# Kernel tuning notes

Hardware: AMD Instinct MI355X
Metric: run time of the kernel (lower is better)

The kernel has to match this reference:

```python
import jax, jax.numpy as jnp
import numpy as np

N_NODES = 100000
N_EDGES = 1600000
NFEAT = 512
HIDDEN = 128
NCLASS = 40


def setup_inputs() -> dict:
    key = jax.random.key(0)
    ks = jax.random.split(key, 8)
    x = jax.random.normal(ks[0], (N_NODES, NFEAT), dtype=jnp.float32)
    edge_src = jax.random.randint(ks[1], (N_EDGES,), 0, N_NODES, dtype=jnp.int32)
    edge_dst = jax.random.randint(ks[2], (N_EDGES,), 0, N_NODES, dtype=jnp.int32)
    # normalized adjacency values (D^-1/2 A D^-1/2 style), all positive
    edge_val = jax.random.uniform(ks[3], (N_EDGES,), dtype=jnp.float32)
    # glorot-ish init like pygcn's reset_parameters
    W1 = jax.random.normal(ks[4], (NFEAT, HIDDEN), dtype=jnp.float32) / np.sqrt(NFEAT)
    b1 = jnp.zeros((HIDDEN,), dtype=jnp.float32)
    W2 = jax.random.normal(ks[5], (HIDDEN, NCLASS), dtype=jnp.float32) / np.sqrt(HIDDEN)
    b2 = jnp.zeros((NCLASS,), dtype=jnp.float32)
    return {"x": x, "edge_src": edge_src, "edge_dst": edge_dst, "edge_val": edge_val,
            "W1": W1, "b1": b1, "W2": W2, "b2": b2}


def _gcn_layer(h, edge_src, edge_dst, edge_val, W, b):
    # support = h @ W ; out = spmm(adj, support) + b
    support = h @ W                                  # [N, d_out]
    msg = support[edge_src] * edge_val[:, None]      # [E, d_out] gather
    agg = jax.ops.segment_sum(msg, edge_dst, num_segments=N_NODES)  # scatter-add
    return agg + b


def reference(x, edge_src, edge_dst, edge_val, W1, b1, W2, b2):
    h = _gcn_layer(x, edge_src, edge_dst, edge_val, W1, b1)
    h = jax.nn.relu(h)
    # dropout=0.0 -> branch skipped (faithful to `if self.dropout:` with falsy value)
    h = _gcn_layer(h, edge_src, edge_dst, edge_val, W2, b2)
    return jax.nn.log_softmax(h, axis=1)
```

## Files before the change

kernel.cpp:

```cpp
#include <hip/hip_runtime.h>
#include <stdint.h>

#define NN 100000
#define NE 1600000
#define NF 512
#define NH 128
#define NC 40
#define BKT 64
#define DEGS 16
#define NGB 782

typedef float f32x4 __attribute__((ext_vector_type(4)));
typedef short bf16x8 __attribute__((ext_vector_type(8)));

__device__ __forceinline__ unsigned short f2bf(float f){
    unsigned u = __float_as_uint(f);
    u = u + 0x7FFFu + ((u >> 16) & 1u);
    return (unsigned short)(u >> 16);
}
__device__ __forceinline__ unsigned pk2(float a, float b){
    return (unsigned)f2bf(a) | ((unsigned)f2bf(b) << 16);
}
__device__ __forceinline__ float blo(unsigned u){ return __uint_as_float(u << 16); }
__device__ __forceinline__ float bhi(unsigned u){ return __uint_as_float(u & 0xffff0000u); }

__global__ __launch_bounds__(256) void wprep(const float* __restrict__ W1, const float* __restrict__ W2,
                                             unsigned short* __restrict__ W1t, unsigned short* __restrict__ W2t){
    int tid = blockIdx.x * 256 + threadIdx.x;
    if (tid < NF * NH){
        int c = tid >> 9;
        int k = tid & 511;
        W1t[c * NF + k] = f2bf(W1[k * NH + c]);
    }
    int t2 = tid - NF * NH;
    if (t2 >= 0 && t2 < 48 * NH){
        int c = t2 >> 7;
        int k = t2 & 127;
        W2t[c * NH + k] = (c < NC) ? f2bf(W2[k * NC + c]) : (unsigned short)0;
    }
}

__global__ __launch_bounds__(256, 3) void gemm1_edge(const float* __restrict__ x,
                                                     const unsigned short* __restrict__ W1t,
                                                     unsigned short* __restrict__ s1,
                                                     const int* __restrict__ esrc,
                                                     const int* __restrict__ edst,
                                                     const float* __restrict__ eval,
                                                     int* __restrict__ deg, int2* __restrict__ pk){
    __shared__ unsigned short Al[2][128 * 40];
    __shared__ unsigned short Bl[2][128 * 40];
    if (blockIdx.x >= NGB){
        int tid = (blockIdx.x - NGB) * 256 + threadIdx.x;
        if (tid < NE){
            int d = edst[tid];
            int pos = atomicAdd(&deg[d * DEGS], 1);
            if (pos < BKT)
                pk[(size_t)d * BKT + pos] = make_int2(esrc[tid], __float_as_int(eval[tid]));
        }
        return;
    }
    const int tid  = threadIdx.x;
    const int wid  = tid >> 6;
    const int lane = tid & 63;
    const int quad = lane >> 4;
    const int l15  = lane & 15;
    const int br   = blockIdx.x * 128;

    const int r    = tid >> 1;
    const int half = tid & 1;

    int arow = br + r; if (arow >= NN) arow = NN - 1;
    const float* aptr = x + (size_t)arow * NF + half * 16;
    const unsigned short* bptr = W1t + (size_t)r * NF + half * 16;

    float4 pa0, pa1, pa2, pa3;
    uint4  pb0, pb1;
    {
        const float4* ap = (const float4*)aptr;
        pa0 = ap[0]; pa1 = ap[1]; pa2 = ap[2]; pa3 = ap[3];
        const uint4* bp = (const uint4*)bptr;
        pb0 = bp[0]; pb1 = bp[1];
        unsigned* Ad = (unsigned*)&Al[0][r * 40 + half * 16];
        Ad[0] = pk2(pa0.x, pa0.y); Ad[1] = pk2(pa0.z, pa0.w);
        Ad[2] = pk2(pa1.x, pa1.y); Ad[3] = pk2(pa1.z, pa1.w);
        Ad[4] = pk2(pa2.x, pa2.y); Ad[5] = pk2(pa2.z, pa2.w);
        Ad[6] = pk2(pa3.x, pa3.y); Ad[7] = pk2(pa3.z, pa3.w);
        uint4* Bd = (uint4*)&Bl[0][r * 40 + half * 16];
        Bd[0] = pb0; Bd[1] = pb1;
    }
    __syncthreads();

    f32x4 acc[2][8];
#pragma unroll
    for (int i = 0; i < 2; i++)
#pragma unroll
        for (int j = 0; j < 8; j++) acc[i][j] = (f32x4){0.f, 0.f, 0.f, 0.f};

    int cur = 0;
    for (int ks = 0; ks < NF; ks += 32){
        const bool more = (ks + 32 < NF);
        if (more){
            const float4* ap = (const float4*)(aptr + ks + 32);
            pa0 = ap[0]; pa1 = ap[1]; pa2 = ap[2]; pa3 = ap[3];
            const uint4* bp = (const uint4*)(bptr + ks + 32);
            pb0 = bp[0]; pb1 = bp[1];
        }

        bf16x8 a0 = *(const bf16x8*)&Al[cur][(wid * 32 +      l15) * 40 + quad * 8];
        bf16x8 a1 = *(const bf16x8*)&Al[cur][(wid * 32 + 16 + l15) * 40 + quad * 8];
        bf16x8 bb[8];
#pragma unroll
        for (int ct = 0; ct < 8; ct++)
            bb[ct] = *(const bf16x8*)&Bl[cur][(ct * 16 + l15) * 40 + quad * 8];
#pragma unroll
        for (int ct = 0; ct < 8; ct++){
            acc[0][ct] = __builtin_amdgcn_mfma_f32_16x16x32_bf16(a0, bb[ct], acc[0][ct], 0, 0, 0);
            acc[1][ct] = __builtin_amdgcn_mfma_f32_16x16x32_bf16(a1, bb[ct], acc[1][ct], 0, 0, 0);
        }

        if (more){
            int nxt = cur ^ 1;
            unsigned* Ad = (unsigned*)&Al[nxt][r * 40 + half * 16];
            Ad[0] = pk2(pa0.x, pa0.y); Ad[1] = pk2(pa0.z, pa0.w);
            Ad[2] = pk2(pa1.x, pa1.y); Ad[3] = pk2(pa1.z, pa1.w);
            Ad[4] = pk2(pa2.x, pa2.y); Ad[5] = pk2(pa2.z, pa2.w);
            Ad[6] = pk2(pa3.x, pa3.y); Ad[7] = pk2(pa3.z, pa3.w);
            uint4* Bd = (uint4*)&Bl[nxt][r * 40 + half * 16];
            Bd[0] = pb0; Bd[1] = pb1;
        }
        __syncthreads();
        cur ^= 1;
    }

#pragma unroll
    for (int rt = 0; rt < 2; rt++)
#pragma unroll
        for (int ct = 0; ct < 8; ct++)
#pragma unroll
            for (int i = 0; i < 4; i++){
                int row = br + wid * 32 + rt * 16 + quad * 4 + i;
                if (row < NN) s1[(size_t)row * NH + ct * 16 + l15] = f2bf(acc[rt][ct][i]);
            }
}

__global__ __launch_bounds__(256) void agg1(const uint4* __restrict__ s1v,
                                            const int* __restrict__ deg,
                                            const int2* __restrict__ pk,
                                            const float* __restrict__ b1, uint4* __restrict__ h){
    const int lane  = threadIdx.x & 63;
    const int quad  = lane >> 4;
    const int hl    = lane & 15;
    const int lbase = quad * 16;
    const int node  = blockIdx.x * 16 + (threadIdx.x >> 6) * 4 + quad;

    const int s = node * BKT;
    int dg = deg[node * DEGS]; if (dg > BKT) dg = BKT;
    const int e = s + dg;
    float a[8];
#pragma unroll
    for (int t = 0; t < 8; t++) a[t] = 0.f;

    int2 rec = make_int2(0, 0);
    {
        int c0 = e - s; if (c0 > 16) c0 = 16;
        if (hl < c0) rec = pk[s + hl];
    }
    for (int base = s; base < e; base += 16){
        int cnt = e - base; if (cnt > 16) cnt = 16;
        int2 cur = rec;
        int nb = base + 16;
        if (nb < e){
            int cn = e - nb; if (cn > 16) cn = 16;
            rec = make_int2(0, 0);
            if (hl < cn) rec = pk[nb + hl];
        }
        int j = 0;
        for (; j + 8 <= cnt; j += 8){
            int is[8];
#pragma unroll
            for (int q = 0; q < 8; q++) is[q] = __shfl(cur.x, lbase + j + q, 64);
            uint4 us[8];
#pragma unroll
            for (int q = 0; q < 8; q++) us[q] = s1v[(size_t)is[q] * 16 + hl];
            float vs[8];
#pragma unroll
            for (int q = 0; q < 8; q++) vs[q] = __int_as_float(__shfl(cur.y, lbase + j + q, 64));
#pragma unroll
            for (int q = 0; q < 8; q++){
                float v = vs[q];
                a[0] += v * blo(us[q].x); a[1] += v * bhi(us[q].x);
                a[2] += v * blo(us[q].y); a[3] += v * bhi(us[q].y);
                a[4] += v * blo(us[q].z); a[5] += v * bhi(us[q].z);
                a[6] += v * blo(us[q].w); a[7] += v * bhi(us[q].w);
            }
        }
        for (; j < cnt; j++){
            int   i0 = __shfl(cur.x, lbase + j, 64);
            float v0 = __int_as_float(__shfl(cur.y, lbase + j, 64));
            uint4 u  = s1v[(size_t)i0 * 16 + hl];
            a[0] += v0 * blo(u.x); a[1] += v0 * bhi(u.x);
            a[2] += v0 * blo(u.y); a[3] += v0 * bhi(u.y);
            a[4] += v0 * blo(u.z); a[5] += v0 * bhi(u.z);
            a[6] += v0 * blo(u.w); a[7] += v0 * bhi(u.w);
        }
    }
    const float4* b1v = (const float4*)b1;
    float4 bA = b1v[2 * hl], bB = b1v[2 * hl + 1];
    a[0] += bA.x; a[1] += bA.y; a[2] += bA.z; a[3] += bA.w;
    a[4] += bB.x; a[5] += bB.y; a[6] += bB.z; a[7] += bB.w;
#pragma unroll
    for (int t = 0; t < 8; t++) a[t] = fmaxf(a[t], 0.f);
    h[(size_t)node * 16 + hl] = make_uint4(pk2(a[0], a[1]), pk2(a[2], a[3]),
                                           pk2(a[4], a[5]), pk2(a[6], a[7]));
}

__global__ __launch_bounds__(256) void gemm2(const unsigned short* __restrict__ h,
                                             const unsigned short* __restrict__ W2t,
                                             unsigned short* __restrict__ s2p){
    const int tid  = threadIdx.x;
    const int wid  = tid >> 6;
    const int lane = tid & 63;
    const int quad = lane >> 4;
    const int l15  = lane & 15;
    const int row0 = blockIdx.x * 64 + wid * 16;

    bf16x8 bf[3][4];
#pragma unroll
    for (int ct = 0; ct < 3; ct++)
#pragma unroll
        for (int ks = 0; ks < 4; ks++)
            bf[ct][ks] = *(const bf16x8*)&W2t[(ct * 16 + l15) * NH + ks * 32 + quad * 8];

    int arow = row0 + l15; if (arow >= NN) arow = NN - 1;
    const unsigned short* ap = h + (size_t)arow * NH;

    bf16x8 a[4];
#pragma unroll
    for (int ks = 0; ks < 4; ks++) a[ks] = *(const bf16x8*)&ap[ks * 32 + quad * 8];

    f32x4 acc[3];
#pragma unroll
    for (int ct = 0; ct < 3; ct++) acc[ct] = (f32x4){0.f, 0.f, 0.f, 0.f};
#pragma unroll
    for (int ks = 0; ks < 4; ks++)
#pragma unroll
        for (int ct = 0; ct < 3; ct++)
            acc[ct] = __builtin_amdgcn_mfma_f32_16x16x32_bf16(a[ks], bf[ct][ks], acc[ct], 0, 0, 0);

#pragma unroll
    for (int ct = 0; ct < 3; ct++)
#pragma unroll
        for (int i = 0; i < 4; i++){
            int row = row0 + quad * 4 + i;
            if (row < NN) s2p[(size_t)row * 64 + ct * 16 + l15] = f2bf(acc[ct][i]);
        }
}

__global__ __launch_bounds__(256) void agg2(const uint4* __restrict__ s2v,
                                            const int* __restrict__ deg,
                                            const int2* __restrict__ pk,
                                            const float* __restrict__ b2, float* __restrict__ out){
    const int lane  = threadIdx.x & 63;
    const int oct   = lane >> 3;
    const int hl    = lane & 7;
    const int lbase = oct * 8;
    const int node  = blockIdx.x * 32 + (threadIdx.x >> 6) * 8 + oct;

    const int s = node * BKT;
    int dg = deg[node * DEGS]; if (dg > BKT) dg = BKT;
    const int e = s + dg;
    float a[8];
#pragma unroll
    for (int t = 0; t < 8; t++) a[t] = 0.f;

    int2 rec = make_int2(0, 0);
    {
        int c0 = e - s; if (c0 > 8) c0 = 8;
        if (hl < c0) rec = pk[s + hl];
    }
    for (int base = s; base < e; base += 8){
        int cnt = e - base; if (cnt > 8) cnt = 8;
        int2 cur = rec;
        int nb = base + 8;
        if (nb < e){
            int cn = e - nb; if (cn > 8) cn = 8;
            rec = make_int2(0, 0);
            if (hl < cn) rec = pk[nb + hl];
        }
        if (cnt == 8){
            int is[8];
#pragma unroll
            for (int q = 0; q < 8; q++) is[q] = __shfl(cur.x, lbase + q, 64);
            uint4 us[8];
#pragma unroll
            for (int q = 0; q < 8; q++) us[q] = s2v[(size_t)is[q] * 8 + hl];
            float vs[8];
#pragma unroll
            for (int q = 0; q < 8; q++) vs[q] = __int_as_float(__shfl(cur.y, lbase + q, 64));
#pragma unroll
            for (int q = 0; q < 8; q++){
                float v = vs[q];
                a[0] += v * blo(us[q].x); a[1] += v * bhi(us[q].x);
                a[2] += v * blo(us[q].y); a[3] += v * bhi(us[q].y);
                a[4] += v * blo(us[q].z); a[5] += v * bhi(us[q].z);
                a[6] += v * blo(us[q].w); a[7] += v * bhi(us[q].w);
            }
        } else {
            for (int j = 0; j < cnt; j++){
                int   i0 = __shfl(cur.x, lbase + j, 64);
                float v0 = __int_as_float(__shfl(cur.y, lbase + j, 64));
                uint4 u  = s2v[(size_t)i0 * 8 + hl];
                a[0] += v0 * blo(u.x); a[1] += v0 * bhi(u.x);
                a[2] += v0 * blo(u.y); a[3] += v0 * bhi(u.y);
                a[4] += v0 * blo(u.z); a[5] += v0 * bhi(u.z);
                a[6] += v0 * blo(u.w); a[7] += v0 * bhi(u.w);
            }
        }
    }
    const bool act = hl < 5;
    float z[8];
    if (act){
        const float4* b2v = (const float4*)b2;
        float4 cA = b2v[2 * hl], cB = b2v[2 * hl + 1];
        z[0] = a[0] + cA.x; z[1] = a[1] + cA.y; z[2] = a[2] + cA.z; z[3] = a[3] + cA.w;
        z[4] = a[4] + cB.x; z[5] = a[5] + cB.y; z[6] = a[6] + cB.z; z[7] = a[7] + cB.w;
    } else {
#pragma unroll
        for (int t = 0; t < 8; t++) z[t] = -INFINITY;
    }
    float m = z[0];
#pragma unroll
    for (int t = 1; t < 8; t++) m = fmaxf(m, z[t]);
#pragma unroll
    for (int o = 4; o; o >>= 1) m = fmaxf(m, __shfl_xor(m, o, 8));
    float pe = 0.f;
    if (act){
#pragma unroll
        for (int t = 0; t < 8; t++) pe += __expf(z[t] - m);
    }
#pragma unroll
    for (int o = 4; o; o >>= 1) pe += __shfl_xor(pe, o, 8);
    if (act){
        float l = __logf(pe) + m;
        float* op = out + (size_t)node * NC + 8 * hl;
        *(float4*)op       = make_float4(z[0] - l, z[1] - l, z[2] - l, z[3] - l);
        *(float4*)(op + 4) = make_float4(z[4] - l, z[5] - l, z[6] - l, z[7] - l);
    }
}

extern "C" void kernel_launch(void* const* d_in, const int* in_sizes, int n_in,
                              void* d_out, int out_size, void* d_ws, size_t ws_size,
                              hipStream_t stream) {
    const float* x    = (const float*)d_in[0];
    const int*   esrc = (const int*)  d_in[1];
    const int*   edst = (const int*)  d_in[2];
    const float* eval = (const float*)d_in[3];
    const float* W1   = (const float*)d_in[4];
    const float* b1   = (const float*)d_in[5];
    const float* W2   = (const float*)d_in[6];
    const float* b2   = (const float*)d_in[7];
    float* out = (float*)d_out;

    char* ws = (char*)d_ws;
    size_t off = 0;
    auto alloc = [&](size_t bytes) -> void* {
        void* p = ws + off;
        off += (bytes + 255) & ~(size_t)255;
        return p;
    };
    unsigned short* W1t  = (unsigned short*)alloc((size_t)NF * NH * 2);
    unsigned short* W2t  = (unsigned short*)alloc((size_t)48 * NH * 2);
    unsigned short* s1   = (unsigned short*)alloc((size_t)NN * NH * 2);
    unsigned short* h    = (unsigned short*)alloc((size_t)NN * NH * 2);
    unsigned short* s2p  = (unsigned short*)alloc((size_t)NN * 64 * 2);
    int*   deg   = (int*)  alloc((size_t)NN * DEGS * 4);
    int2*  pk    = (int2*) alloc((size_t)NN * BKT * 8);

    hipMemsetAsync(deg, 0, (size_t)NN * DEGS * 4, stream);

    wprep     <<<280, 256, 0, stream>>>(W1, W2, W1t, W2t);
    gemm1_edge<<<NGB + (NE + 255) / 256, 256, 0, stream>>>(x, W1t, s1, esrc, edst, eval, deg, pk);
    agg1      <<<NN / 16, 256, 0, stream>>>((const uint4*)s1, deg, pk, b1, (uint4*)h);
    gemm2     <<<(NN + 63) / 64, 256, 0, stream>>>(h, W2t, s2p);
    agg2      <<<NN / 32, 256, 0, stream>>>((const uint4*)s2p, deg, pk, b2, out);
}
```

Measured before the change: 501.6 us.

## Fuse layer-1 aggregation with layer-2 GEMM through shared memory

Merges the agg1 and gemm2 kernels. Each block now aggregates 64 nodes in four passes, keeps the ReLU'd bf16 hidden rows in an LDS tile, and then runs the MFMA projection against W2 directly from that tile. This drops the global write and re-read of the 100000x128 hidden matrix and one kernel launch. In exchange, blocks cover 4x more nodes, so there are fewer blocks and less parallelism for the latency-bound gather, plus a block barrier before the GEMM.

```diff
diff --git a/kernel.cpp b/kernel.cpp
--- a/kernel.cpp
+++ b/kernel.cpp
@@ -143,100 +143,102 @@
             }
 }
 
-__global__ __launch_bounds__(256) void agg1(const uint4* __restrict__ s1v,
-                                            const int* __restrict__ deg,
-                                            const int2* __restrict__ pk,
-                                            const float* __restrict__ b1, uint4* __restrict__ h){
-    const int lane  = threadIdx.x & 63;
+__global__ __launch_bounds__(256) void agg1g2(const uint4* __restrict__ s1v,
+                                              const int* __restrict__ deg,
+                                              const int2* __restrict__ pk,
+                                              const float* __restrict__ b1,
+                                              const unsigned short* __restrict__ W2t,
+                                              unsigned short* __restrict__ s2p){
+    __shared__ unsigned short Hl[64][136];
+    const int tid   = threadIdx.x;
+    const int wid   = tid >> 6;
+    const int lane  = tid & 63;
     const int quad  = lane >> 4;
     const int hl    = lane & 15;
     const int lbase = quad * 16;
-    const int node  = blockIdx.x * 16 + (threadIdx.x >> 6) * 4 + quad;
-
-    const int s = node * BKT;
-    int dg = deg[node * DEGS]; if (dg > BKT) dg = BKT;
-    const int e = s + dg;
-    float a[8];
-#pragma unroll
-    for (int t = 0; t < 8; t++) a[t] = 0.f;
-
-    int2 rec = make_int2(0, 0);
-    {
-        int c0 = e - s; if (c0 > 16) c0 = 16;
-        if (hl < c0) rec = pk[s + hl];
-    }
-    for (int base = s; base < e; base += 16){
-        int cnt = e - base; if (cnt > 16) cnt = 16;
-        int2 cur = rec;
-        int nb = base + 16;
-        if (nb < e){
-            int cn = e - nb; if (cn > 16) cn = 16;
-            rec = make_int2(0, 0);
-            if (hl < cn) rec = pk[nb + hl];
-        }
-        int j = 0;
-        for (; j + 8 <= cnt; j += 8){
-            int is[8];
-#pragma unroll
-            for (int q = 0; q < 8; q++) is[q] = __shfl(cur.x, lbase + j + q, 64);
-            uint4 us[8];
-#pragma unroll
-            for (int q = 0; q < 8; q++) us[q] = s1v[(size_t)is[q] * 16 + hl];
-            float vs[8];
-#pragma unroll
-            for (int q = 0; q < 8; q++) vs[q] = __int_as_float(__shfl(cur.y, lbase + j + q, 64));
-#pragma unroll
-            for (int q = 0; q < 8; q++){
-                float v = vs[q];
-                a[0] += v * blo(us[q].x); a[1] += v * bhi(us[q].x);
-                a[2] += v * blo(us[q].y); a[3] += v * bhi(us[q].y);
-                a[4] += v * blo(us[q].z); a[5] += v * bhi(us[q].z);
-                a[6] += v * blo(us[q].w); a[7] += v * bhi(us[q].w);
-            }
-        }
-        for (; j < cnt; j++){
-            int   i0 = __shfl(cur.x, lbase + j, 64);
-            float v0 = __int_as_float(__shfl(cur.y, lbase + j, 64));
-            uint4 u  = s1v[(size_t)i0 * 16 + hl];
-            a[0] += v0 * blo(u.x); a[1] += v0 * bhi(u.x);
-            a[2] += v0 * blo(u.y); a[3] += v0 * bhi(u.y);
-            a[4] += v0 * blo(u.z); a[5] += v0 * bhi(u.z);
-            a[6] += v0 * blo(u.w); a[7] += v0 * bhi(u.w);
-        }
-    }
+    const int nb    = blockIdx.x * 64;
+
     const float4* b1v = (const float4*)b1;
-    float4 bA = b1v[2 * hl], bB = b1v[2 * hl + 1];
-    a[0] += bA.x; a[1] += bA.y; a[2] += bA.z; a[3] += bA.w;
-    a[4] += bB.x; a[5] += bB.y; a[6] += bB.z; a[7] += bB.w;
-#pragma unroll
-    for (int t = 0; t < 8; t++) a[t] = fmaxf(a[t], 0.f);
-    h[(size_t)node * 16 + hl] = make_uint4(pk2(a[0], a[1]), pk2(a[2], a[3]),
-                                           pk2(a[4], a[5]), pk2(a[6], a[7]));
-}
-
-__global__ __launch_bounds__(256) void gemm2(const unsigned short* __restrict__ h,
-                                             const unsigned short* __restrict__ W2t,
-                                             unsigned short* __restrict__ s2p){
-    const int tid  = threadIdx.x;
-    const int wid  = tid >> 6;
-    const int lane = tid & 63;
-    const int quad = lane >> 4;
-    const int l15  = lane & 15;
-    const int row0 = blockIdx.x * 64 + wid * 16;
+    const float4 bA = b1v[2 * hl], bB = b1v[2 * hl + 1];
+
+#pragma unroll
+    for (int pass = 0; pass < 4; pass++){
+        const int nloc = pass * 16 + wid * 4 + quad;
+        const int node = nb + nloc;
+        float a[8];
+#pragma unroll
+        for (int t = 0; t < 8; t++) a[t] = 0.f;
+
+        if (node < NN){
+            const int s = node * BKT;
+            int dg = deg[node * DEGS]; if (dg > BKT) dg = BKT;
+            const int e = s + dg;
+
+            int2 rec = make_int2(0, 0);
+            {
+                int c0 = e - s; if (c0 > 16) c0 = 16;
+                if (hl < c0) rec = pk[s + hl];
+            }
+            for (int base = s; base < e; base += 16){
+                int cnt = e - base; if (cnt > 16) cnt = 16;
+                int2 cur = rec;
+                int nxb = base + 16;
+                if (nxb < e){
+                    int cn = e - nxb; if (cn > 16) cn = 16;
+                    rec = make_int2(0, 0);
+                    if (hl < cn) rec = pk[nxb + hl];
+                }
+                int j = 0;
+                for (; j + 8 <= cnt; j += 8){
+                    int is[8];
+#pragma unroll
+                    for (int q = 0; q < 8; q++) is[q] = __shfl(cur.x, lbase + j + q, 64);
+                    uint4 us[8];
+#pragma unroll
+                    for (int q = 0; q < 8; q++) us[q] = s1v[(size_t)is[q] * 16 + hl];
+                    float vs[8];
+#pragma unroll
+                    for (int q = 0; q < 8; q++) vs[q] = __int_as_float(__shfl(cur.y, lbase + j + q, 64));
+#pragma unroll
+                    for (int q = 0; q < 8; q++){
+                        float v = vs[q];
+                        a[0] += v * blo(us[q].x); a[1] += v * bhi(us[q].x);
+                        a[2] += v * blo(us[q].y); a[3] += v * bhi(us[q].y);
+                        a[4] += v * blo(us[q].z); a[5] += v * bhi(us[q].z);
+                        a[6] += v * blo(us[q].w); a[7] += v * bhi(us[q].w);
+                    }
+                }
+                for (; j < cnt; j++){
+                    int   i0 = __shfl(cur.x, lbase + j, 64);
+                    float v0 = __int_as_float(__shfl(cur.y, lbase + j, 64));
+                    uint4 u  = s1v[(size_t)i0 * 16 + hl];
+                    a[0] += v0 * blo(u.x); a[1] += v0 * bhi(u.x);
+                    a[2] += v0 * blo(u.y); a[3] += v0 * bhi(u.y);
+                    a[4] += v0 * blo(u.z); a[5] += v0 * bhi(u.z);
+                    a[6] += v0 * blo(u.w); a[7] += v0 * bhi(u.w);
+                }
+            }
+            a[0] += bA.x; a[1] += bA.y; a[2] += bA.z; a[3] += bA.w;
+            a[4] += bB.x; a[5] += bB.y; a[6] += bB.z; a[7] += bB.w;
+#pragma unroll
+            for (int t = 0; t < 8; t++) a[t] = fmaxf(a[t], 0.f);
+        }
+        *(uint4*)&Hl[nloc][hl * 8] = make_uint4(pk2(a[0], a[1]), pk2(a[2], a[3]),
+                                                pk2(a[4], a[5]), pk2(a[6], a[7]));
+    }
+    __syncthreads();
 
     bf16x8 bf[3][4];
 #pragma unroll
     for (int ct = 0; ct < 3; ct++)
 #pragma unroll
         for (int ks = 0; ks < 4; ks++)
-            bf[ct][ks] = *(const bf16x8*)&W2t[(ct * 16 + l15) * NH + ks * 32 + quad * 8];
-
-    int arow = row0 + l15; if (arow >= NN) arow = NN - 1;
-    const unsigned short* ap = h + (size_t)arow * NH;
-
-    bf16x8 a[4];
-#pragma unroll
-    for (int ks = 0; ks < 4; ks++) a[ks] = *(const bf16x8*)&ap[ks * 32 + quad * 8];
+            bf[ct][ks] = *(const bf16x8*)&W2t[(ct * 16 + hl) * NH + ks * 32 + quad * 8];
+
+    bf16x8 af[4];
+#pragma unroll
+    for (int ks = 0; ks < 4; ks++)
+        af[ks] = *(const bf16x8*)&Hl[wid * 16 + hl][ks * 32 + quad * 8];
 
     f32x4 acc[3];
 #pragma unroll
@@ -245,14 +247,14 @@
     for (int ks = 0; ks < 4; ks++)
 #pragma unroll
         for (int ct = 0; ct < 3; ct++)
-            acc[ct] = __builtin_amdgcn_mfma_f32_16x16x32_bf16(a[ks], bf[ct][ks], acc[ct], 0, 0, 0);
+            acc[ct] = __builtin_amdgcn_mfma_f32_16x16x32_bf16(af[ks], bf[ct][ks], acc[ct], 0, 0, 0);
 
 #pragma unroll
     for (int ct = 0; ct < 3; ct++)
 #pragma unroll
         for (int i = 0; i < 4; i++){
-            int row = row0 + quad * 4 + i;
-            if (row < NN) s2p[(size_t)row * 64 + ct * 16 + l15] = f2bf(acc[ct][i]);
+            int row = nb + wid * 16 + quad * 4 + i;
+            if (row < NN) s2p[(size_t)row * 64 + ct * 16 + hl] = f2bf(acc[ct][i]);
         }
 }
 
@@ -371,7 +373,6 @@
     unsigned short* W1t  = (unsigned short*)alloc((size_t)NF * NH * 2);
     unsigned short* W2t  = (unsigned short*)alloc((size_t)48 * NH * 2);
     unsigned short* s1   = (unsigned short*)alloc((size_t)NN * NH * 2);
-    unsigned short* h    = (unsigned short*)alloc((size_t)NN * NH * 2);
     unsigned short* s2p  = (unsigned short*)alloc((size_t)NN * 64 * 2);
     int*   deg   = (int*)  alloc((size_t)NN * DEGS * 4);
     int2*  pk    = (int2*) alloc((size_t)NN * BKT * 8);
@@ -380,7 +381,6 @@
 
     wprep     <<<280, 256, 0, stream>>>(W1, W2, W1t, W2t);
     gemm1_edge<<<NGB + (NE + 255) / 256, 256, 0, stream>>>(x, W1t, s1, esrc, edst, eval, deg, pk);
-    agg1      <<<NN / 16, 256, 0, stream>>>((const uint4*)s1, deg, pk, b1, (uint4*)h);
-    gemm2     <<<(NN + 63) / 64, 256, 0, stream>>>(h, W2t, s2p);
+    agg1g2    <<<(NN + 63) / 64, 256, 0, stream>>>((const uint4*)s1, deg, pk, b1, W2t, s2p);
     agg2      <<<NN / 32, 256, 0, stream>>>((const uint4*)s2p, deg, pk, b2, out);
 }
```

Result: no change. 505.7 us (+0.8%).
